# Kernel tuning notes

Hardware: AMD Instinct MI355X
Metric: run time of the kernel (lower is better)

The kernel has to match this reference:

```python
import jax, jax.numpy as jnp
import numpy as np

B, T, C, H = 4, 2048, 768, 12
D = C // H  # head dim = 64

def setup_inputs() -> dict:
    key = jax.random.key(0)
    k1, k2, k3, k4, k5 = jax.random.split(key, 5)
    s = 0.02
    x = jax.random.normal(k1, (B, T, C), dtype=jnp.float32)
    w_qkv = jax.random.normal(k2, (3 * C, C), dtype=jnp.float32) * s  # torch Linear weight [out,in]
    b_qkv = jax.random.normal(k3, (3 * C,), dtype=jnp.float32) * s
    w_proj = jax.random.normal(k4, (C, C), dtype=jnp.float32) * s
    b_proj = jax.random.normal(k5, (C,), dtype=jnp.float32) * s
    return {"x": x, "w_qkv": w_qkv, "b_qkv": b_qkv, "w_proj": w_proj, "b_proj": b_proj}

def reference(x, w_qkv, b_qkv, w_proj, b_proj):
    Bx, Tx, Cx = x.shape
    # qkv projection: torch Linear y = x @ W.T + b
    qkv = x @ w_qkv.T + b_qkv                      # [B,T,3C]
    qkv = qkv.reshape(Bx, Tx, 3, H, D)
    q, k, v = qkv[:, :, 0], qkv[:, :, 1], qkv[:, :, 2]  # each [B,T,H,D]
    scale = 1.0 / jnp.sqrt(jnp.float32(D))
    scores = jnp.einsum('bqhd,bkhd->bhqk', q, k) * scale  # [B,H,T,T]
    causal = jnp.tril(jnp.ones((Tx, Tx), dtype=bool))
    scores = jnp.where(causal[None, None], scores, -jnp.inf)
    attn = jax.nn.softmax(scores, axis=-1)
    out = jnp.einsum('bhqk,bkhd->bqhd', attn, v).reshape(Bx, Tx, Cx)
    return out @ w_proj.T + b_proj
```

## Files before the change

### kernel.cpp

```cpp
#include <hip/hip_runtime.h>
#include <hip/hip_bf16.h>
#include <cstdint>
#include <cstddef>

typedef __bf16 bf16_t;
typedef __bf16 bf16x8 __attribute__((ext_vector_type(8)));
typedef __bf16 bf16x4 __attribute__((ext_vector_type(4)));
typedef float f32x4 __attribute__((ext_vector_type(4)));
typedef float f32x16 __attribute__((ext_vector_type(16)));

constexpr int B_ = 4, T_ = 2048, C_ = 768, H_ = 12, D_ = 64;
constexpr size_t QKV_ELEMS = (size_t)B_ * H_ * T_ * D_;

__device__ __forceinline__ void gload16(const bf16_t* g, bf16_t* l) {
    __builtin_amdgcn_global_load_lds(
        (const __attribute__((address_space(1))) unsigned int*)g,
        (__attribute__((address_space(3))) unsigned int*)l, 16, 0, 0);
}

__global__ __launch_bounds__(256)
void conv_bf16(const float* __restrict__ a, bf16_t* __restrict__ oa, int na8,
               const float* __restrict__ b, bf16_t* __restrict__ ob, int nb8)
{
    int i = blockIdx.x * 256 + threadIdx.x;
    if (i >= na8 + nb8) return;
    const float* src; bf16_t* dst; int idx;
    if (i < na8) { src = a; dst = oa; idx = i; }
    else         { src = b; dst = ob; idx = i - na8; }
    const float4* p = reinterpret_cast<const float4*>(src + (size_t)idx * 8);
    float4 f0 = p[0], f1 = p[1];
    bf16x8 t;
    t[0]=(bf16_t)f0.x; t[1]=(bf16_t)f0.y; t[2]=(bf16_t)f0.z; t[3]=(bf16_t)f0.w;
    t[4]=(bf16_t)f1.x; t[5]=(bf16_t)f1.y; t[6]=(bf16_t)f1.z; t[7]=(bf16_t)f1.w;
    *reinterpret_cast<bf16x8*>(dst + (size_t)idx * 8) = t;
}

__global__ __launch_bounds__(256, 3)
void qkv_gemm(const bf16_t* __restrict__ xb, const bf16_t* __restrict__ wb,
              const float* __restrict__ bias,
              bf16_t* __restrict__ q, bf16_t* __restrict__ k, bf16_t* __restrict__ v)
{
    __shared__ alignas(16) bf16_t As[128 * 64];
    __shared__ alignas(16) bf16_t Bs[128 * 64];
    const int tid  = threadIdx.x;
    const int lane = tid & 63;
    const int w    = tid >> 6;
    const int wm = w >> 1, wn = w & 1;
    const int bm = blockIdx.x & 63;
    const int bn = blockIdx.x >> 6;
    const int m0 = bm * 128, n0 = bn * 128;
    const int lcol = lane & 15, lgrp = lane >> 4;
    const int srow = lane >> 3;
    const int scol = ((lane & 7) ^ srow) * 8;

    const bf16_t* ag = xb + (size_t)(m0 + w * 32 + srow) * C_ + scol;
    const bf16_t* bg = wb + (size_t)(n0 + w * 32 + srow) * C_ + scol;
    bf16_t* al = &As[(w * 32) * 64];
    bf16_t* bl = &Bs[(w * 32) * 64];

    f32x4 acc[4][4] = {};

    for (int kt = 0; kt < C_; kt += 64) {
        __syncthreads();
        #pragma unroll
        for (int p = 0; p < 4; ++p) {
            gload16(ag + (size_t)(p * 8) * C_ + kt, al + p * 8 * 64);
            gload16(bg + (size_t)(p * 8) * C_ + kt, bl + p * 8 * 64);
        }
        __syncthreads();
        #pragma unroll
        for (int kk = 0; kk < 2; ++kk) {
            bf16x8 af[4], bfr[4];
            #pragma unroll
            for (int i = 0; i < 4; ++i) {
                const int R = wm * 64 + i * 16 + lcol;
                af[i] = *reinterpret_cast<const bf16x8*>(&As[R * 64 + (((kk*4 + lgrp) ^ (R & 7)) << 3)]);
            }
            #pragma unroll
            for (int j = 0; j < 4; ++j) {
                const int R = wn * 64 + j * 16 + lcol;
                bfr[j] = *reinterpret_cast<const bf16x8*>(&Bs[R * 64 + (((kk*4 + lgrp) ^ (R & 7)) << 3)]);
            }
            #pragma unroll
            for (int i = 0; i < 4; ++i)
                #pragma unroll
                for (int j = 0; j < 4; ++j)
                    acc[i][j] = __builtin_amdgcn_mfma_f32_16x16x32_bf16(af[i], bfr[j], acc[i][j], 0, 0, 0);
        }
    }

    #pragma unroll
    for (int j = 0; j < 4; ++j) {
        const int n = n0 + wn * 64 + j * 16 + lcol;
        const float bv = bias[n];
        const int s = n / C_, rem = n % C_;
        const int h = rem >> 6, d = rem & 63;
        bf16_t* dst = (s == 0) ? q : (s == 1) ? k : v;
        #pragma unroll
        for (int i = 0; i < 4; ++i) {
            #pragma unroll
            for (int r = 0; r < 4; ++r) {
                const int m = m0 + wm * 64 + i * 16 + lgrp * 4 + r;
                const int b = m >> 11, t = m & (T_ - 1);
                dst[(((size_t)(b * H_ + h)) * T_ + t) * D_ + d] = (bf16_t)(acc[i][j][r] + bv);
            }
        }
    }
}

__global__ __launch_bounds__(256, 2)
void attn_fwd(const bf16_t* __restrict__ qg, const bf16_t* __restrict__ kg,
              const bf16_t* __restrict__ vg, bf16_t* __restrict__ og)
{
    __shared__ alignas(16) bf16_t Ks[2 * 64 * 64];
    __shared__ alignas(16) bf16_t Vt[2 * 64 * 64];

    const int tid  = threadIdx.x;
    const int lane = tid & 63;
    const int w    = tid >> 6;
    const int l31  = lane & 31;
    const int hi   = lane >> 5;
    const int qi   = blockIdx.x / 48;
    const int bh   = blockIdx.x % 48;
    const int qt   = 15 - qi;
    const int q0   = qt * 128;
    const int qw   = q0 + w * 32;
    const size_t base = (size_t)bh * T_ * D_;
    const int qrow = qw + l31;

    const float SCL = 0.125f * 1.44269504f;
    bf16x8 bq[4];
    #pragma unroll
    for (int kt = 0; kt < 4; ++kt) {
        bf16x8 t = *reinterpret_cast<const bf16x8*>(qg + base + (size_t)qrow * D_ + kt*16 + hi*8);
        #pragma unroll
        for (int e = 0; e < 8; ++e) t[e] = (bf16_t)((float)t[e] * SCL);
        bq[kt] = t;
    }

    f32x16 ot0 = {};
    f32x16 ot1 = {};
    float m = -1e30f, rowl = 0.0f;

    const int skey = tid >> 3;
    const int sgr  = tid & 7;
    const int va_  = tid >> 3;
    const bf16_t* srcK = kg + base + (size_t)skey * D_ + sgr * 8;
    const bf16_t* srcV = vg + base + (size_t)(2 * va_) * D_ + sgr * 8;

    union U8 { bf16x8 v; uint32_t u[4]; };
    U8 kr0, kr1, vr0, vr1;

    kr0.v = *reinterpret_cast<const bf16x8*>(srcK);
    kr1.v = *reinterpret_cast<const bf16x8*>(srcK + (size_t)32 * D_);
    vr0.v = *reinterpret_cast<const bf16x8*>(srcV);
    vr1.v = *reinterpret_cast<const bf16x8*>(srcV + D_);
    {
        *reinterpret_cast<bf16x8*>(Ks + skey * 64 + ((sgr ^ (skey & 7)) << 3)) = kr0.v;
        *reinterpret_cast<bf16x8*>(Ks + (32 + skey) * 64 + ((sgr ^ (skey & 7)) << 3)) = kr1.v;
        #pragma unroll
        for (int j = 0; j < 8; ++j) {
            const int d = sgr * 8 + j;
            const int ss = ((va_ >> 2) ^ j ^ sgr) & 7;
            uint32_t wd = __builtin_amdgcn_perm(vr1.u[j >> 1], vr0.u[j >> 1],
                                                (j & 1) ? 0x07060302u : 0x05040100u);
            *reinterpret_cast<uint32_t*>(Vt + d * 64 + ss * 8 + (va_ & 3) * 2) = wd;
        }
    }

    const int ntiles = qt * 2 + 2;
    for (int it = 0; it < ntiles; ++it) {
        const int off  = (it & 1) << 12;
        const int offn = off ^ 4096;
        __syncthreads();

        const bool pre = (it + 1 < ntiles);
        if (pre) {
            const size_t soff = (size_t)(it + 1) * 64 * D_;
            kr0.v = *reinterpret_cast<const bf16x8*>(srcK + soff);
            kr1.v = *reinterpret_cast<const bf16x8*>(srcK + soff + (size_t)32 * D_);
            vr0.v = *reinterpret_cast<const bf16x8*>(srcV + soff);
            vr1.v = *reinterpret_cast<const bf16x8*>(srcV + soff + D_);
        }

        const int kv0 = it * 64;
        #pragma unroll
        for (int sk = 0; sk < 2; ++sk) {
            const int kvs = kv0 + sk * 32;
            if (kvs > qw + 31) continue;

            f32x16 s = {};
            __builtin_amdgcn_s_setprio(1);
            #pragma unroll
            for (int kt = 0; kt < 4; ++kt) {
                const int keyl = sk * 32 + l31;
                const int slot = kt * 2 + hi;
                bf16x8 ka = *reinterpret_cast<const bf16x8*>(
                    Ks + off + keyl * 64 + ((slot ^ (keyl & 7)) << 3));
                s = __builtin_amdgcn_mfma_f32_32x32x16_bf16(ka, bq[kt], s, 0, 0, 0);
            }
            __builtin_amdgcn_s_setprio(0);
            if (kvs + 31 > qw) {
                #pragma unroll
                for (int r = 0; r < 16; ++r) {
                    const int key = kvs + (r & 3) + 8 * (r >> 2) + 4 * hi;
                    if (key > qrow) s[r] = -1e30f;
                }
            }
            float a0 = fmaxf(fmaxf(s[0],  s[1]),  s[2]);
            float a1 = fmaxf(fmaxf(s[3],  s[4]),  s[5]);
            float a2 = fmaxf(fmaxf(s[6],  s[7]),  s[8]);
            float a3 = fmaxf(fmaxf(s[9],  s[10]), s[11]);
            float a4 = fmaxf(fmaxf(s[12], s[13]), s[14]);
            float b0 = fmaxf(fmaxf(a0, a1), a2);
            float b1 = fmaxf(fmaxf(a3, a4), s[15]);
            float mt = fmaxf(b0, b1);
            mt = fmaxf(mt, __shfl_xor(mt, 32));
            if (!__all(mt <= m + 8.0f)) {
                const float mnew = fmaxf(m, mt);
                const float alpha = exp2f(m - mnew);
                #pragma unroll
                for (int r = 0; r < 16; ++r) { ot0[r] *= alpha; ot1[r] *= alpha; }
                rowl *= alpha;
                m = mnew;
            }
            #pragma unroll
            for (int r = 0; r < 16; ++r) s[r] = exp2f(s[r] - m);
            float t0 = (s[0]+s[1]) + (s[2]+s[3]);
            float t1 = (s[4]+s[5]) + (s[6]+s[7]);
            float t2 = (s[8]+s[9]) + (s[10]+s[11]);
            float t3 = (s[12]+s[13]) + (s[14]+s[15]);
            float rs = (t0 + t1) + (t2 + t3);
            rs += __shfl_xor(rs, 32);
            rowl += rs;

            uint32_t c0, c1, c2, c3, c4, c5, c6, c7;
            asm("v_cvt_pk_bf16_f32 %0, %1, %2" : "=v"(c0) : "v"(s[0]),  "v"(s[1]));
            asm("v_cvt_pk_bf16_f32 %0, %1, %2" : "=v"(c1) : "v"(s[2]),  "v"(s[3]));
            asm("v_cvt_pk_bf16_f32 %0, %1, %2" : "=v"(c2) : "v"(s[4]),  "v"(s[5]));
            asm("v_cvt_pk_bf16_f32 %0, %1, %2" : "=v"(c3) : "v"(s[6]),  "v"(s[7]));
            asm("v_cvt_pk_bf16_f32 %0, %1, %2" : "=v"(c4) : "v"(s[8]),  "v"(s[9]));
            asm("v_cvt_pk_bf16_f32 %0, %1, %2" : "=v"(c5) : "v"(s[10]), "v"(s[11]));
            asm("v_cvt_pk_bf16_f32 %0, %1, %2" : "=v"(c6) : "v"(s[12]), "v"(s[13]));
            asm("v_cvt_pk_bf16_f32 %0, %1, %2" : "=v"(c7) : "v"(s[14]), "v"(s[15]));
            asm("v_permlane32_swap_b32 %0, %1" : "+v"(c0), "+v"(c2));
            asm("v_permlane32_swap_b32 %0, %1" : "+v"(c1), "+v"(c3));
            asm("v_permlane32_swap_b32 %0, %1" : "+v"(c4), "+v"(c6));
            asm("v_permlane32_swap_b32 %0, %1" : "+v"(c5), "+v"(c7));
            union U { uint32_t u[4]; bf16x8 v; };
            U pa0; pa0.u[0] = c0; pa0.u[1] = c1; pa0.u[2] = c2; pa0.u[3] = c3;
            U pa1; pa1.u[0] = c4; pa1.u[1] = c5; pa1.u[2] = c6; pa1.u[3] = c7;

            __builtin_amdgcn_s_setprio(1);
            #pragma unroll
            for (int dblk = 0; dblk < 2; ++dblk) {
                const int d = dblk * 32 + l31;
                f32x16& o = dblk ? ot1 : ot0;
                #pragma unroll
                for (int ktile = 0; ktile < 2; ++ktile) {
                    const int kslot = sk * 4 + ktile * 2 + hi;
                    const int ss = kslot ^ (d & 7) ^ ((d >> 3) & 7);
                    bf16x8 va = *reinterpret_cast<const bf16x8*>(Vt + off + d * 64 + (ss << 3));
                    o = __builtin_amdgcn_mfma_f32_32x32x16_bf16(va, ktile ? pa1.v : pa0.v, o, 0, 0, 0);
                }
            }
            __builtin_amdgcn_s_setprio(0);
        }

        if (pre) {
            *reinterpret_cast<bf16x8*>(Ks + offn + skey * 64 + ((sgr ^ (skey & 7)) << 3)) = kr0.v;
            *reinterpret_cast<bf16x8*>(Ks + offn + (32 + skey) * 64 + ((sgr ^ (skey & 7)) << 3)) = kr1.v;
            #pragma unroll
            for (int j = 0; j < 8; ++j) {
                const int d = sgr * 8 + j;
                const int ss = ((va_ >> 2) ^ j ^ sgr) & 7;
                uint32_t wd = __builtin_amdgcn_perm(vr1.u[j >> 1], vr0.u[j >> 1],
                                                    (j & 1) ? 0x07060302u : 0x05040100u);
                *reinterpret_cast<uint32_t*>(Vt + offn + d * 64 + ss * 8 + (va_ & 3) * 2) = wd;
            }
        }
    }

    const int b = bh / H_, h = bh % H_;
    const float inv = 1.0f / rowl;
    bf16_t* dst = &og[((size_t)b * T_ + qrow) * C_ + h * D_];
    #pragma unroll
    for (int dblk = 0; dblk < 2; ++dblk) {
        const f32x16& o = dblk ? ot1 : ot0;
        #pragma unroll
        for (int qd = 0; qd < 4; ++qd) {
            bf16x4 v4;
            #pragma unroll
            for (int r = 0; r < 4; ++r) v4[r] = (bf16_t)(o[qd * 4 + r] * inv);
            *reinterpret_cast<bf16x4*>(dst + dblk * 32 + qd * 8 + hi * 4) = v4;
        }
    }
}

__global__ __launch_bounds__(256, 3)
void proj_gemm(const bf16_t* __restrict__ ao, const bf16_t* __restrict__ wpb,
               const float* __restrict__ bias, float* __restrict__ out)
{
    __shared__ alignas(16) bf16_t As[128 * 64];
    __shared__ alignas(16) bf16_t Bs[128 * 64];
    const int tid  = threadIdx.x;
    const int lane = tid & 63;
    const int w    = tid >> 6;
    const int wm = w >> 1, wn = w & 1;
    const int bm = blockIdx.x & 63;
    const int bn = blockIdx.x >> 6;
    const int m0 = bm * 128, n0 = bn * 128;
    const int lcol = lane & 15, lgrp = lane >> 4;
    const int srow = lane >> 3;
    const int scol = ((lane & 7) ^ srow) * 8;

    const bf16_t* ag = ao  + (size_t)(m0 + w * 32 + srow) * C_ + scol;
    const bf16_t* bg = wpb + (size_t)(n0 + w * 32 + srow) * C_ + scol;
    bf16_t* al = &As[(w * 32) * 64];
    bf16_t* bl = &Bs[(w * 32) * 64];

    f32x4 acc[4][4] = {};

    for (int kt = 0; kt < C_; kt += 64) {
        __syncthreads();
        #pragma unroll
        for (int p = 0; p < 4; ++p) {
            gload16(ag + (size_t)(p * 8) * C_ + kt, al + p * 8 * 64);
            gload16(bg + (size_t)(p * 8) * C_ + kt, bl + p * 8 * 64);
        }
        __syncthreads();
        #pragma unroll
        for (int kk = 0; kk < 2; ++kk) {
            bf16x8 af[4], bfr[4];
            #pragma unroll
            for (int i = 0; i < 4; ++i) {
                const int R = wm * 64 + i * 16 + lcol;
                af[i] = *reinterpret_cast<const bf16x8*>(&As[R * 64 + (((kk*4 + lgrp) ^ (R & 7)) << 3)]);
            }
            #pragma unroll
            for (int j = 0; j < 4; ++j) {
                const int R = wn * 64 + j * 16 + lcol;
                bfr[j] = *reinterpret_cast<const bf16x8*>(&Bs[R * 64 + (((kk*4 + lgrp) ^ (R & 7)) << 3)]);
            }
            #pragma unroll
            for (int i = 0; i < 4; ++i)
                #pragma unroll
                for (int j = 0; j < 4; ++j)
                    acc[i][j] = __builtin_amdgcn_mfma_f32_16x16x32_bf16(af[i], bfr[j], acc[i][j], 0, 0, 0);
        }
    }

    #pragma unroll
    for (int j = 0; j < 4; ++j) {
        const int n = n0 + wn * 64 + j * 16 + lcol;
        const float bv = bias[n];
        #pragma unroll
        for (int i = 0; i < 4; ++i) {
            #pragma unroll
            for (int r = 0; r < 4; ++r) {
                const int m = m0 + wm * 64 + i * 16 + lgrp * 4 + r;
                out[(size_t)m * C_ + n] = acc[i][j][r] + bv;
            }
        }
    }
}

extern "C" void kernel_launch(void* const* d_in, const int* in_sizes, int n_in,
                              void* d_out, int out_size, void* d_ws, size_t ws_size,
                              hipStream_t stream)
{
    const float* x      = (const float*)d_in[0];
    const float* w_qkv  = (const float*)d_in[1];
    const float* b_qkv  = (const float*)d_in[2];
    const float* w_proj = (const float*)d_in[3];
    const float* b_proj = (const float*)d_in[4];
    float* out = (float*)d_out;

    bf16_t* ws = (bf16_t*)d_ws;
    bf16_t* q   = ws;
    bf16_t* k   = ws +     QKV_ELEMS;
    bf16_t* v   = ws + 2 * QKV_ELEMS;
    bf16_t* ao  = ws + 3 * QKV_ELEMS;
    bf16_t* xb  = ao;
    bf16_t* wqb = (bf16_t*)d_out;
    bf16_t* wpb = k;

    conv_bf16<<<dim3(3936), 256, 0, stream>>>(x, xb, 786432, w_qkv, wqb, 221184);
    qkv_gemm<<<dim3(64 * 18), 256, 0, stream>>>(xb, wqb, b_qkv, q, k, v);
    attn_fwd<<<dim3(16 * 48), 256, 0, stream>>>(q, k, v, ao);
    conv_bf16<<<dim3(288), 256, 0, stream>>>(w_proj, wpb, 73728, w_proj, wpb, 0);
    proj_gemm<<<dim3(64 * 6), 256, 0, stream>>>(ao, wpb, b_proj, out);
}
```

Measured before the change: 124.0 us.

## Shrink attention blocks to 64 query rows with single-buffered K/V tiles

The attention kernel now runs 128-thread blocks covering 64 query rows (two waves) instead of 256-thread blocks covering 128 rows, doubling the grid. K/V shared memory drops from double to single buffering, with an extra barrier per tile; the next tile's global loads are still issued into registers before compute. This aims for finer causal load balance and more resident blocks per CU. In exchange each K/V tile is loaded by twice as many blocks, and the shared-memory write now sits between two barriers instead of overlapping with compute.

Measured after the change: 135.3 us. 9.1% more time.

```diff
diff --git a/kernel.cpp b/kernel.cpp
--- a/kernel.cpp
+++ b/kernel.cpp
@@ -108,12 +108,12 @@
     }
 }
 
-__global__ __launch_bounds__(256, 2)
+__global__ __launch_bounds__(128, 3)
 void attn_fwd(const bf16_t* __restrict__ qg, const bf16_t* __restrict__ kg,
               const bf16_t* __restrict__ vg, bf16_t* __restrict__ og)
 {
-    __shared__ alignas(16) bf16_t Ks[2 * 64 * 64];
-    __shared__ alignas(16) bf16_t Vt[2 * 64 * 64];
+    __shared__ alignas(16) bf16_t Ks[64 * 64];
+    __shared__ alignas(16) bf16_t Vt[64 * 64];
 
     const int tid  = threadIdx.x;
     const int lane = tid & 63;
@@ -122,8 +122,8 @@
     const int hi   = lane >> 5;
     const int qi   = blockIdx.x / 48;
     const int bh   = blockIdx.x % 48;
-    const int qt   = 15 - qi;
-    const int q0   = qt * 128;
+    const int qt   = 31 - qi;
+    const int q0   = qt * 64;
     const int qw   = q0 + w * 32;
     const size_t base = (size_t)bh * T_ * D_;
     const int qrow = qw + l31;
@@ -144,50 +144,61 @@
 
     const int skey = tid >> 3;
     const int sgr  = tid & 7;
-    const int va_  = tid >> 3;
     const bf16_t* srcK = kg + base + (size_t)skey * D_ + sgr * 8;
-    const bf16_t* srcV = vg + base + (size_t)(2 * va_) * D_ + sgr * 8;
+    const bf16_t* srcV = vg + base + (size_t)(2 * skey) * D_ + sgr * 8;
 
     union U8 { bf16x8 v; uint32_t u[4]; };
-    U8 kr0, kr1, vr0, vr1;
-
-    kr0.v = *reinterpret_cast<const bf16x8*>(srcK);
-    kr1.v = *reinterpret_cast<const bf16x8*>(srcK + (size_t)32 * D_);
-    vr0.v = *reinterpret_cast<const bf16x8*>(srcV);
-    vr1.v = *reinterpret_cast<const bf16x8*>(srcV + D_);
-    {
-        *reinterpret_cast<bf16x8*>(Ks + skey * 64 + ((sgr ^ (skey & 7)) << 3)) = kr0.v;
-        *reinterpret_cast<bf16x8*>(Ks + (32 + skey) * 64 + ((sgr ^ (skey & 7)) << 3)) = kr1.v;
-        #pragma unroll
-        for (int j = 0; j < 8; ++j) {
-            const int d = sgr * 8 + j;
-            const int ss = ((va_ >> 2) ^ j ^ sgr) & 7;
-            uint32_t wd = __builtin_amdgcn_perm(vr1.u[j >> 1], vr0.u[j >> 1],
-                                                (j & 1) ? 0x07060302u : 0x05040100u);
-            *reinterpret_cast<uint32_t*>(Vt + d * 64 + ss * 8 + (va_ & 3) * 2) = wd;
-        }
-    }
-
-    const int ntiles = qt * 2 + 2;
+    U8 kr[4], vr[2][2];
+
+    #pragma unroll
+    for (int p = 0; p < 4; ++p)
+        kr[p].v = *reinterpret_cast<const bf16x8*>(srcK + (size_t)(p * 16) * D_);
+    #pragma unroll
+    for (int p = 0; p < 2; ++p) {
+        vr[p][0].v = *reinterpret_cast<const bf16x8*>(srcV + (size_t)(p * 32) * D_);
+        vr[p][1].v = *reinterpret_cast<const bf16x8*>(srcV + (size_t)(p * 32 + 1) * D_);
+    }
+
+    union UP { uint32_t u[4]; bf16x8 v; };
+
+    const int ntiles = qt + 1;
     for (int it = 0; it < ntiles; ++it) {
-        const int off  = (it & 1) << 12;
-        const int offn = off ^ 4096;
-        __syncthreads();
-
-        const bool pre = (it + 1 < ntiles);
-        if (pre) {
+        __syncthreads();
+        #pragma unroll
+        for (int p = 0; p < 4; ++p) {
+            const int key = p * 16 + skey;
+            *reinterpret_cast<bf16x8*>(Ks + key * 64 + ((sgr ^ (key & 7)) << 3)) = kr[p].v;
+        }
+        #pragma unroll
+        for (int p = 0; p < 2; ++p) {
+            const int va = p * 16 + skey;
+            #pragma unroll
+            for (int j = 0; j < 8; ++j) {
+                const int d = sgr * 8 + j;
+                const int ss = ((va >> 2) ^ j ^ sgr) & 7;
+                uint32_t wd = __builtin_amdgcn_perm(vr[p][1].u[j >> 1], vr[p][0].u[j >> 1],
+                                                    (j & 1) ? 0x07060302u : 0x05040100u);
+                *reinterpret_cast<uint32_t*>(Vt + d * 64 + ss * 8 + (va & 3) * 2) = wd;
+            }
+        }
+        __syncthreads();
+        if (it + 1 < ntiles) {
             const size_t soff = (size_t)(it + 1) * 64 * D_;
-            kr0.v = *reinterpret_cast<const bf16x8*>(srcK + soff);
-            kr1.v = *reinterpret_cast<const bf16x8*>(srcK + soff + (size_t)32 * D_);
-            vr0.v = *reinterpret_cast<const bf16x8*>(srcV + soff);
-            vr1.v = *reinterpret_cast<const bf16x8*>(srcV + soff + D_);
+            #pragma unroll
+            for (int p = 0; p < 4; ++p)
+                kr[p].v = *reinterpret_cast<const bf16x8*>(srcK + soff + (size_t)(p * 16) * D_);
+            #pragma unroll
+            for (int p = 0; p < 2; ++p) {
+                vr[p][0].v = *reinterpret_cast<const bf16x8*>(srcV + soff + (size_t)(p * 32) * D_);
+                vr[p][1].v = *reinterpret_cast<const bf16x8*>(srcV + soff + (size_t)(p * 32 + 1) * D_);
+            }
         }
 
         const int kv0 = it * 64;
         #pragma unroll
         for (int sk = 0; sk < 2; ++sk) {
             const int kvs = kv0 + sk * 32;
-            if (kvs > qw + 31) continue;
+            if (sk == 1 && kvs > qw + 31) continue;
 
             f32x16 s = {};
             __builtin_amdgcn_s_setprio(1);
@@ -196,7 +207,7 @@
                 const int keyl = sk * 32 + l31;
                 const int slot = kt * 2 + hi;
                 bf16x8 ka = *reinterpret_cast<const bf16x8*>(
-                    Ks + off + keyl * 64 + ((slot ^ (keyl & 7)) << 3));
+                    Ks + keyl * 64 + ((slot ^ (keyl & 7)) << 3));
                 s = __builtin_amdgcn_mfma_f32_32x32x16_bf16(ka, bq[kt], s, 0, 0, 0);
             }
             __builtin_amdgcn_s_setprio(0);
@@ -247,9 +258,8 @@
             asm("v_permlane32_swap_b32 %0, %1" : "+v"(c1), "+v"(c3));
             asm("v_permlane32_swap_b32 %0, %1" : "+v"(c4), "+v"(c6));
             asm("v_permlane32_swap_b32 %0, %1" : "+v"(c5), "+v"(c7));
-            union U { uint32_t u[4]; bf16x8 v; };
-            U pa0; pa0.u[0] = c0; pa0.u[1] = c1; pa0.u[2] = c2; pa0.u[3] = c3;
-            U pa1; pa1.u[0] = c4; pa1.u[1] = c5; pa1.u[2] = c6; pa1.u[3] = c7;
+            UP pa0; pa0.u[0] = c0; pa0.u[1] = c1; pa0.u[2] = c2; pa0.u[3] = c3;
+            UP pa1; pa1.u[0] = c4; pa1.u[1] = c5; pa1.u[2] = c6; pa1.u[3] = c7;
 
             __builtin_amdgcn_s_setprio(1);
             #pragma unroll
@@ -260,24 +270,11 @@
                 for (int ktile = 0; ktile < 2; ++ktile) {
                     const int kslot = sk * 4 + ktile * 2 + hi;
                     const int ss = kslot ^ (d & 7) ^ ((d >> 3) & 7);
-                    bf16x8 va = *reinterpret_cast<const bf16x8*>(Vt + off + d * 64 + (ss << 3));
+                    bf16x8 va = *reinterpret_cast<const bf16x8*>(Vt + d * 64 + (ss << 3));
                     o = __builtin_amdgcn_mfma_f32_32x32x16_bf16(va, ktile ? pa1.v : pa0.v, o, 0, 0, 0);
                 }
             }
             __builtin_amdgcn_s_setprio(0);
-        }
-
-        if (pre) {
-            *reinterpret_cast<bf16x8*>(Ks + offn + skey * 64 + ((sgr ^ (skey & 7)) << 3)) = kr0.v;
-            *reinterpret_cast<bf16x8*>(Ks + offn + (32 + skey) * 64 + ((sgr ^ (skey & 7)) << 3)) = kr1.v;
-            #pragma unroll
-            for (int j = 0; j < 8; ++j) {
-                const int d = sgr * 8 + j;
-                const int ss = ((va_ >> 2) ^ j ^ sgr) & 7;
-                uint32_t wd = __builtin_amdgcn_perm(vr1.u[j >> 1], vr0.u[j >> 1],
-                                                    (j & 1) ? 0x07060302u : 0x05040100u);
-                *reinterpret_cast<uint32_t*>(Vt + offn + d * 64 + ss * 8 + (va_ & 3) * 2) = wd;
-            }
         }
     }
 
@@ -387,7 +384,7 @@
 
     conv_bf16<<<dim3(3936), 256, 0, stream>>>(x, xb, 786432, w_qkv, wqb, 221184);
     qkv_gemm<<<dim3(64 * 18), 256, 0, stream>>>(xb, wqb, b_qkv, q, k, v);
-    attn_fwd<<<dim3(16 * 48), 256, 0, stream>>>(q, k, v, ao);
+    attn_fwd<<<dim3(32 * 48), 128, 0, stream>>>(q, k, v, ao);
     conv_bf16<<<dim3(288), 256, 0, stream>>>(w_proj, wpb, 73728, w_proj, wpb, 0);
     proj_gemm<<<dim3(64 * 6), 256, 0, stream>>>(ao, wpb, b_proj, out);
 }
```
